# Kernel optimization log

Hardware: AMD Instinct MI355X
Metric: run time of the kernel (lower is better)

Reference implementation:

```python
import jax, jax.numpy as jnp
import numpy as np

NC, NX, NY = 32, 512, 512
N_LOC = 100000


def setup_inputs() -> dict:
    key = jax.random.key(0)
    k1, k2 = jax.random.split(key)
    x = jax.random.normal(k1, (8, NC, NX, NY), dtype=jnp.float32)
    kernel = jnp.zeros((1, NC, NX, NY), dtype=jnp.float32)
    variable_kernel = jax.random.normal(k2, (N_LOC,), dtype=jnp.float32)
    # unique flat indices into the (NC, NX, NY) kernel volume (cluster locations)
    rng = np.random.default_rng(0)
    loc_idx = jnp.asarray(rng.choice(NC * NX * NY, N_LOC, replace=False).astype(np.int64))
    return {"x": x, "kernel": kernel, "variable_kernel": variable_kernel, "loc_idx": loc_idx}


def fill_kernel(kernel, variable_kernel, loc_idx):
    # scatter ReLU'd trainable values into the sparse PSF locations
    k0 = kernel[0].reshape(-1).at[loc_idx].set(jax.nn.relu(variable_kernel))
    return k0.reshape(NC, NX, NY)


def disperse_all_orders(x, k):
    # per-channel circular convolution with the multi-order dispersion PSF,
    # summed over spectral channels onto the sensor: (b, nx, ny)
    Xf = jnp.fft.rfft2(x, axes=(-2, -1))          # (b, nc, nx, ny//2+1)
    Kf = jnp.fft.rfft2(k, axes=(-2, -1))          # (nc, nx, ny//2+1)
    Yf = jnp.sum(Xf * Kf[None], axis=1)           # (b, nx, ny//2+1)
    return jnp.fft.irfft2(Yf, s=(NX, NY), axes=(-2, -1))


def reference(x, kernel, variable_kernel, loc_idx):
    k = fill_kernel(kernel, variable_kernel, loc_idx)
    return disperse_all_orders(x, k)
```

## Files before the change

### kernel.cpp

```cpp
#include <hip/hip_runtime.h>
#include <cstdint>

#define NXX 512
#define NYY 512
#define NCH 32
#define NB  8
#define NU  257
#define IMG_CPLX (NU*NXX)
#define PIX (NXX*NYY)

__device__ __forceinline__ uint32_t f2bf(float f){
  uint32_t u = __float_as_uint(f);
  return (u + 0x7FFFu + ((u >> 16) & 1u)) >> 16;
}
__device__ __forceinline__ float bf2f(uint32_t h){ return __uint_as_float(h << 16); }
__device__ __forceinline__ uint32_t packbf(float re, float im){ return f2bf(re) | (f2bf(im) << 16); }

#define WAIT_LGKM() asm volatile("s_waitcnt lgkmcnt(0)" ::: "memory")

__device__ __forceinline__ void cmul(float& zr, float& zi, float wr, float wi){
  float r = zr*wr - zi*wi;
  zi = zr*wi + zi*wr;
  zr = r;
}

template<int DIR>
__device__ __forceinline__ void bfly8(float* xr, float* xi){
  const float S = 0.70710678118654752440f;
  float er0=xr[0]+xr[4], ei0=xi[0]+xi[4];
  float er1=xr[1]+xr[5], ei1=xi[1]+xi[5];
  float er2=xr[2]+xr[6], ei2=xi[2]+xi[6];
  float er3=xr[3]+xr[7], ei3=xi[3]+xi[7];
  float or0=xr[0]-xr[4], oi0=xi[0]-xi[4];
  float or1=xr[1]-xr[5], oi1=xi[1]-xi[5];
  float or2=xr[2]-xr[6], oi2=xi[2]-xi[6];
  float or3=xr[3]-xr[7], oi3=xi[3]-xi[7];
  float p0r=er0+er2, p0i=ei0+ei2;
  float p1r=er0-er2, p1i=ei0-ei2;
  float q0r=er1+er3, q0i=ei1+ei3;
  float q1r=er1-er3, q1i=ei1-ei3;
  float w4r, w4i;
  if (DIR<0){ w4r=q1i; w4i=-q1r; } else { w4r=-q1i; w4i=q1r; }
  xr[0]=p0r+q0r; xi[0]=p0i+q0i;
  xr[4]=p0r-q0r; xi[4]=p0i-q0i;
  xr[2]=p1r+w4r; xi[2]=p1i+w4i;
  xr[6]=p1r-w4r; xi[6]=p1i-w4i;
  float f1r,f1i,f2r,f2i,f3r,f3i;
  if (DIR<0){
    f1r=S*(or1+oi1); f1i=S*(oi1-or1);
    f2r=oi2;         f2i=-or2;
    f3r=S*(oi3-or3); f3i=-S*(or3+oi3);
  } else {
    f1r=S*(or1-oi1);  f1i=S*(or1+oi1);
    f2r=-oi2;         f2i=or2;
    f3r=-S*(or3+oi3); f3i=S*(or3-oi3);
  }
  float g0r=or0+f2r, g0i=oi0+f2i;
  float g1r=or0-f2r, g1i=oi0-f2i;
  float h0r=f1r+f3r, h0i=f1i+f3i;
  float h1r=f1r-f3r, h1i=f1i-f3i;
  float v4r, v4i;
  if (DIR<0){ v4r=h1i; v4i=-h1r; } else { v4r=-h1i; v4i=h1r; }
  xr[1]=g0r+h0r; xi[1]=g0i+h0i;
  xr[5]=g0r-h0r; xi[5]=g0i-h0i;
  xr[3]=g1r+v4r; xi[3]=g1i+v4i;
  xr[7]=g1r-v4r; xi[7]=g1i-v4i;
}

__device__ __forceinline__ void make_tw(int t, float* t1r, float* t1i, float* t2r, float* t2i){
  const float TP = 6.283185307179586476925f;
  float s, c;
  sincosf(-TP * (float)t * (1.0f/512.0f), &s, &c);
  t1r[0]=1.0f; t1i[0]=0.0f;
  #pragma unroll
  for (int k=1;k<8;k++){ t1r[k]=t1r[k-1]*c - t1i[k-1]*s; t1i[k]=t1r[k-1]*s + t1i[k-1]*c; }
  sincosf(-TP * (float)(t>>3) * (1.0f/64.0f), &s, &c);
  t2r[0]=1.0f; t2i[0]=0.0f;
  #pragma unroll
  for (int k=1;k<8;k++){ t2r[k]=t2r[k-1]*c - t2i[k-1]*s; t2i[k]=t2r[k-1]*s + t2i[k-1]*c; }
}

template<int DIR>
__device__ __forceinline__ void fft512(float* ar, float* ai, float* sre, float* sim, int t,
    const float* t1r, const float* t1i, const float* t2r, const float* t2i){
  bfly8<DIR>(ar, ai);
  #pragma unroll
  for (int k=1;k<8;k++){ cmul(ar[k], ai[k], t1r[k], (DIR<0)? t1i[k] : -t1i[k]); }
  #pragma unroll
  for (int k=0;k<8;k++){ int d = 8*t + k; d += (d>>5); sre[d]=ar[k]; sim[d]=ai[k]; }
  WAIT_LGKM();
  #pragma unroll
  for (int j=0;j<8;j++){ int s2 = t + (j<<6); s2 += (s2>>5); ar[j]=sre[s2]; ai[j]=sim[s2]; }
  WAIT_LGKM();
  bfly8<DIR>(ar, ai);
  #pragma unroll
  for (int k=1;k<8;k++){ cmul(ar[k], ai[k], t2r[k], (DIR<0)? t2i[k] : -t2i[k]); }
  #pragma unroll
  for (int k=0;k<8;k++){ int d = (t&7) + ((t>>3)<<6) + (k<<3); d += (d>>5); sre[d]=ar[k]; sim[d]=ai[k]; }
  WAIT_LGKM();
  #pragma unroll
  for (int j=0;j<8;j++){ int s2 = t + (j<<6); s2 += (s2>>5); ar[j]=sre[s2]; ai[j]=sim[s2]; }
  WAIT_LGKM();
  bfly8<DIR>(ar, ai);
}

__device__ __forceinline__ void stage_col_bf16(const uint32_t* __restrict__ col, float* S, int t,
                                               float* ar, float* ai){
  const uint4* c4 = (const uint4*)col;
  uint4 a = c4[t], b = c4[64+t];
  uint32_t wa[4]={a.x,a.y,a.z,a.w}, wb[4]={b.x,b.y,b.z,b.w};
  #pragma unroll
  for (int q=0;q<4;q++){
    int e=4*t+q,   d =e +(e >>5);  S[d ]=__uint_as_float(wa[q]);
    int e2=e+256,  d2=e2+(e2>>5);  S[d2]=__uint_as_float(wb[q]);
  }
  WAIT_LGKM();
  #pragma unroll
  for (int j=0;j<8;j++){ int s2=t+(j<<6); s2+=(s2>>5);
    uint32_t v=__float_as_uint(S[s2]); ar[j]=bf2f(v&0xFFFFu); ai[j]=bf2f(v>>16); }
  WAIT_LGKM();
}

__global__ __launch_bounds__(256) void k_zero(uint4* __restrict__ p, int n4){
  int stride = gridDim.x * 256;
  for (int i = blockIdx.x*256 + threadIdx.x; i < n4; i += stride)
    p[i] = make_uint4(0u,0u,0u,0u);
}

__global__ void k_scatter(const float* __restrict__ vk, const int* __restrict__ loc,
                          uint16_t* __restrict__ kbuf, int n){
  int i = blockIdx.x*256 + threadIdx.x;
  if (i < n){ float v = vk[i]; v = v > 0.0f ? v : 0.0f; kbuf[loc[i]] = (uint16_t)f2bf(v); }
}

template<int BF16>
__global__ __launch_bounds__(512) void k_p1(const void* __restrict__ srcv,
                                            uint32_t* __restrict__ dst){
  __shared__ float sre[8][528], sim[8][528];
  __shared__ uint32_t staged[NU*33];
  const int tid = threadIdx.x;
  const int w = tid >> 6, t = tid & 63;
  const int img = blockIdx.x >> 4;
  const int rblock = (blockIdx.x & 15) << 5;
  float t1r[8],t1i[8],t2r[8],t2i[8];
  make_tw(t, t1r,t1i,t2r,t2i);
  float* S = sre[w];
  float* T = sim[w];
  #pragma unroll
  for (int p=0; p<2; p++){
    const int il = (w<<2) + (p<<1);
    float ar[8], ai[8];
    if (BF16){
      const uint16_t* base = (const uint16_t*)srcv + (size_t)img*PIX + (size_t)(rblock + il)*NYY;
      const uint4* A4 = (const uint4*)base;
      uint4 a = A4[t], b = A4[64+t];
      uint32_t wa[4]={a.x,a.y,a.z,a.w}, wb[4]={b.x,b.y,b.z,b.w};
      #pragma unroll
      for (int q=0;q<4;q++){
        int e0=8*t+2*q, e1=e0+1;
        int d0=e0+(e0>>5), d1=e1+(e1>>5);
        S[d0]=bf2f(wa[q]&0xFFFFu); S[d1]=bf2f(wa[q]>>16);
        T[d0]=bf2f(wb[q]&0xFFFFu); T[d1]=bf2f(wb[q]>>16);
      }
      WAIT_LGKM();
      #pragma unroll
      for (int j=0;j<8;j++){ int s2=t+(j<<6); s2+=(s2>>5); ar[j]=S[s2]; ai[j]=T[s2]; }
      WAIT_LGKM();
    } else {
      const float* rowA = (const float*)srcv + (size_t)img*PIX + (size_t)(rblock + il)*NYY;
      const float4* A4 = (const float4*)rowA;
      float4 a0=A4[t], a1=A4[64+t], b0=A4[128+t], b1=A4[192+t];
      ((float4*)S)[t]=a0; ((float4*)S)[64+t]=a1;
      ((float4*)T)[t]=b0; ((float4*)T)[64+t]=b1;
      WAIT_LGKM();
      #pragma unroll
      for (int j=0;j<8;j++){ ar[j]=S[t+(j<<6)]; ai[j]=T[t+(j<<6)]; }
      WAIT_LGKM();
    }
    fft512<-1>(ar,ai,S,T,t,t1r,t1i,t2r,t2i);
    #pragma unroll
    for (int k=0;k<8;k++){ int d = t+(k<<6); d += (d>>5); S[d]=ar[k]; T[d]=ai[k]; }
    WAIT_LGKM();
    #pragma unroll
    for (int k=0;k<5;k++){
      int u = t + (k<<6);
      if (u < NU){
        int e2 = (512 - u) & 511;
        int du = u + (u>>5), d2 = e2 + (e2>>5);
        float zur=S[du], zui=T[du];
        float zvr=S[d2], zvi=T[d2];
        float Ar=0.5f*(zur+zvr), Ai=0.5f*(zui-zvi);
        float Br=0.5f*(zui+zvi), Bi=0.5f*(zvr-zur);
        staged[u*33 + il]     = packbf(Ar,Ai);
        staged[u*33 + il + 1] = packbf(Br,Bi);
      }
    }
    WAIT_LGKM();
  }
  __syncthreads();
  uint32_t* ob = dst + (size_t)img*IMG_CPLX;
  for (int e = tid; e < NU*32; e += 512){
    int u = e >> 5, il2 = e & 31;
    ob[(size_t)u*NXX + rblock + il2] = staged[u*33 + il2];
  }
}

__global__ __launch_bounds__(512) void k_p2k(uint32_t* __restrict__ rtk){
  __shared__ float sre[8][528], sim[8][528];
  const int w = threadIdx.x >> 6, t = threadIdx.x & 63;
  const int fid = blockIdx.x*8 + w;
  const int c = fid / NU, u = fid % NU;
  float t1r[8],t1i[8],t2r[8],t2i[8];
  make_tw(t, t1r,t1i,t2r,t2i);
  uint32_t* col = rtk + (size_t)c*IMG_CPLX + (size_t)u*NXX;
  float ar[8], ai[8];
  stage_col_bf16(col, sre[w], t, ar, ai);
  fft512<-1>(ar,ai,sre[w],sim[w],t,t1r,t1i,t2r,t2i);
  #pragma unroll
  for (int k=0;k<8;k++){ col[t+(k<<6)] = packbf(ar[k], ai[k]); }
}

__global__ __launch_bounds__(512) void k_p3(const uint32_t* __restrict__ rtx,
    const uint32_t* __restrict__ rtk, uint32_t* __restrict__ y3, int b0, int gsh){
  __shared__ float sre[8][528], sim[8][528];
  __shared__ float redr[8][512], redi[8][512];
  const int tid = threadIdx.x;
  const int w = tid >> 6, t = tid & 63;
  const int u  = blockIdx.x >> gsh;
  const int bl = blockIdx.x & ((1<<gsh)-1);
  float t1r[8],t1i[8],t2r[8],t2i[8];
  make_tw(t, t1r,t1i,t2r,t2i);
  float accr[8], acci[8];
  #pragma unroll
  for (int k=0;k<8;k++){ accr[k]=0.0f; acci[k]=0.0f; }
  #pragma unroll
  for (int cc=0; cc<4; cc++){
    const int c = (w<<2) + cc;
    const uint32_t* xc = rtx + ((size_t)(bl*NCH + c))*IMG_CPLX + (size_t)u*NXX;
    const uint32_t* kc = rtk + (size_t)c*IMG_CPLX + (size_t)u*NXX;
    uint32_t kv[8];
    #pragma unroll
    for (int j=0;j<8;j++){ kv[j]=kc[t+(j<<6)]; }
    float ar[8], ai[8];
    stage_col_bf16(xc, sre[w], t, ar, ai);
    fft512<-1>(ar,ai,sre[w],sim[w],t,t1r,t1i,t2r,t2i);
    #pragma unroll
    for (int k=0;k<8;k++){
      float kr=bf2f(kv[k] & 0xFFFFu), ki=bf2f(kv[k] >> 16);
      accr[k] += ar[k]*kr - ai[k]*ki;
      acci[k] += ar[k]*ki + ai[k]*kr;
    }
  }
  #pragma unroll
  for (int k=0;k<8;k++){ redr[w][t+(k<<6)] = accr[k]; redi[w][t+(k<<6)] = acci[k]; }
  __syncthreads();
  const float sc = 1.0f/262144.0f;
  float sr=0.0f, si=0.0f;
  #pragma unroll
  for (int ww=0; ww<8; ww++){ sr += redr[ww][tid]; si += redi[ww][tid]; }
  redr[0][tid] = sr*sc; redi[0][tid] = si*sc;
  __syncthreads();
  if (w==0){
    float ar[8], ai[8];
    #pragma unroll
    for (int j=0;j<8;j++){ ar[j]=redr[0][t+(j<<6)]; ai[j]=redi[0][t+(j<<6)]; }
    fft512<1>(ar,ai,sre[0],sim[0],t,t1r,t1i,t2r,t2i);
    uint32_t* yc = y3 + ((size_t)(b0+bl)*NU + u)*NXX;
    #pragma unroll
    for (int k=0;k<8;k++){ yc[t+(k<<6)] = packbf(ar[k], ai[k]); }
  }
}

__global__ __launch_bounds__(512) void k_p4(const uint32_t* __restrict__ y3,
                                            float* __restrict__ out){
  __shared__ float sre[8][528], sim[8][528];
  __shared__ uint32_t sta[NU*17];
  const int tid = threadIdx.x, w = tid>>6, t = tid&63;
  const int b = blockIdx.x >> 5;
  const int i0 = (blockIdx.x & 31) << 4;
  const uint32_t* yb = y3 + (size_t)b*IMG_CPLX;
  for (int e = tid; e < NU*16; e += 512){
    int u = e >> 4, il = e & 15;
    sta[u*17 + il] = yb[(size_t)u*NXX + i0 + il];
  }
  __syncthreads();
  float t1r[8],t1i[8],t2r[8],t2i[8];
  make_tw(t, t1r,t1i,t2r,t2i);
  float ar[8], ai[8];
  #pragma unroll
  for (int j=0;j<8;j++){
    int e = t + (j<<6);
    if (e <= 256){
      uint32_t pa_ = sta[e*17 + 2*w], pb_ = sta[e*17 + 2*w + 1];
      float Ar=bf2f(pa_&0xFFFFu), Ai=bf2f(pa_>>16);
      float Br=bf2f(pb_&0xFFFFu), Bi=bf2f(pb_>>16);
      ar[j] = Ar - Bi; ai[j] = Ai + Br;
    } else {
      int ep = 512 - e;
      uint32_t pa_ = sta[ep*17 + 2*w], pb_ = sta[ep*17 + 2*w + 1];
      float Ar=bf2f(pa_&0xFFFFu), Ai=bf2f(pa_>>16);
      float Br=bf2f(pb_&0xFFFFu), Bi=bf2f(pb_>>16);
      ar[j] = Ar + Bi; ai[j] = Br - Ai;
    }
  }
  fft512<1>(ar,ai,sre[w],sim[w],t,t1r,t1i,t2r,t2i);
  float* ob = out + (size_t)b*PIX + (size_t)(i0 + 2*w)*NYY;
  #pragma unroll
  for (int k=0;k<8;k++){ int n = t+(k<<6); ob[n]=ar[k]; ob[NYY+n]=ai[k]; }
}

extern "C" void kernel_launch(void* const* d_in, const int* in_sizes, int n_in,
                              void* d_out, int out_size, void* d_ws, size_t ws_size,
                              hipStream_t stream) {
  const float* x  = (const float*)d_in[0];
  const float* vk = (const float*)d_in[2];
  const int*   loc= (const int*)d_in[3];
  float* out = (float*)d_out;
  char* ws = (char*)d_ws;
  const int n_loc = in_sizes[2];

  const size_t kbytes16 = (size_t)NCH*PIX*2;
  const size_t imgbytes = (size_t)IMG_CPLX*4;

  uint16_t* kbuf = (uint16_t*)ws;
  uint32_t* y3   = (uint32_t*)ws;
  uint32_t* rtk  = (uint32_t*)(ws + kbytes16);
  uint32_t* rtx  = rtk + (size_t)NCH*IMG_CPLX;

  int G = 8;
  while (G > 1 && kbytes16 + (size_t)(NCH + NCH*G)*imgbytes > ws_size) G >>= 1;
  const int gsh = (G==8)?3:((G==4)?2:((G==2)?1:0));

  k_zero<<<2048, 256, 0, stream>>>((uint4*)kbuf, (int)(kbytes16/16));
  k_scatter<<<(n_loc+255)/256, 256, 0, stream>>>(vk, loc, kbuf, n_loc);
  k_p1<1><<<NCH*16, 512, 0, stream>>>(kbuf, rtk);
  k_p2k<<<(NCH*NU)/8, 512, 0, stream>>>(rtk);
  for (int b0 = 0; b0 < NB; b0 += G){
    k_p1<0><<<G*NCH*16, 512, 0, stream>>>(x + (size_t)b0*NCH*PIX, rtx);
    k_p3<<<NU<<gsh, 512, 0, stream>>>(rtx, rtk, y3, b0, gsh);
  }
  k_p4<<<NB*32, 512, 0, stream>>>(y3, out);
}
```

Measured before the change: 196.5 us.

## Load FFT inputs directly from global memory and shrink batch group size

Replaces the LDS staging of input rows and columns (vectorized global load, shared-memory write, then strided read) with direct strided global loads into registers in k_p1, k_p2k and k_p3. This removes LDS round trips and their waitcnt barriers, but the global loads become less vectorized and less coalesced. The batch group G drops from 8 to 2, so the p1/p3 pair runs four times over a smaller workspace. That may keep intermediates cache-resident, at the cost of more launches and lower per-launch parallelism.

```diff
diff --git a/kernel.cpp b/kernel.cpp
--- a/kernel.cpp
+++ b/kernel.cpp
@@ -104,23 +104,6 @@
   bfly8<DIR>(ar, ai);
 }
 
-__device__ __forceinline__ void stage_col_bf16(const uint32_t* __restrict__ col, float* S, int t,
-                                               float* ar, float* ai){
-  const uint4* c4 = (const uint4*)col;
-  uint4 a = c4[t], b = c4[64+t];
-  uint32_t wa[4]={a.x,a.y,a.z,a.w}, wb[4]={b.x,b.y,b.z,b.w};
-  #pragma unroll
-  for (int q=0;q<4;q++){
-    int e=4*t+q,   d =e +(e >>5);  S[d ]=__uint_as_float(wa[q]);
-    int e2=e+256,  d2=e2+(e2>>5);  S[d2]=__uint_as_float(wb[q]);
-  }
-  WAIT_LGKM();
-  #pragma unroll
-  for (int j=0;j<8;j++){ int s2=t+(j<<6); s2+=(s2>>5);
-    uint32_t v=__float_as_uint(S[s2]); ar[j]=bf2f(v&0xFFFFu); ai[j]=bf2f(v>>16); }
-  WAIT_LGKM();
-}
-
 __global__ __launch_bounds__(256) void k_zero(uint4* __restrict__ p, int n4){
   int stride = gridDim.x * 256;
   for (int i = blockIdx.x*256 + threadIdx.x; i < n4; i += stride)
@@ -168,14 +151,8 @@
       WAIT_LGKM();
     } else {
       const float* rowA = (const float*)srcv + (size_t)img*PIX + (size_t)(rblock + il)*NYY;
-      const float4* A4 = (const float4*)rowA;
-      float4 a0=A4[t], a1=A4[64+t], b0=A4[128+t], b1=A4[192+t];
-      ((float4*)S)[t]=a0; ((float4*)S)[64+t]=a1;
-      ((float4*)T)[t]=b0; ((float4*)T)[64+t]=b1;
-      WAIT_LGKM();
       #pragma unroll
-      for (int j=0;j<8;j++){ ar[j]=S[t+(j<<6)]; ai[j]=T[t+(j<<6)]; }
-      WAIT_LGKM();
+      for (int j=0;j<8;j++){ ar[j]=rowA[t+(j<<6)]; ai[j]=rowA[NYY + t + (j<<6)]; }
     }
     fft512<-1>(ar,ai,S,T,t,t1r,t1i,t2r,t2i);
     #pragma unroll
@@ -214,7 +191,8 @@
   make_tw(t, t1r,t1i,t2r,t2i);
   uint32_t* col = rtk + (size_t)c*IMG_CPLX + (size_t)u*NXX;
   float ar[8], ai[8];
-  stage_col_bf16(col, sre[w], t, ar, ai);
+  #pragma unroll
+  for (int j=0;j<8;j++){ uint32_t v = col[t+(j<<6)]; ar[j]=bf2f(v & 0xFFFFu); ai[j]=bf2f(v >> 16); }
   fft512<-1>(ar,ai,sre[w],sim[w],t,t1r,t1i,t2r,t2i);
   #pragma unroll
   for (int k=0;k<8;k++){ col[t+(k<<6)] = packbf(ar[k], ai[k]); }
@@ -238,11 +216,12 @@
     const int c = (w<<2) + cc;
     const uint32_t* xc = rtx + ((size_t)(bl*NCH + c))*IMG_CPLX + (size_t)u*NXX;
     const uint32_t* kc = rtk + (size_t)c*IMG_CPLX + (size_t)u*NXX;
-    uint32_t kv[8];
-    #pragma unroll
-    for (int j=0;j<8;j++){ kv[j]=kc[t+(j<<6)]; }
+    uint32_t xv[8], kv[8];
+    #pragma unroll
+    for (int j=0;j<8;j++){ xv[j]=xc[t+(j<<6)]; kv[j]=kc[t+(j<<6)]; }
     float ar[8], ai[8];
-    stage_col_bf16(xc, sre[w], t, ar, ai);
+    #pragma unroll
+    for (int j=0;j<8;j++){ ar[j]=bf2f(xv[j] & 0xFFFFu); ai[j]=bf2f(xv[j] >> 16); }
     fft512<-1>(ar,ai,sre[w],sim[w],t,t1r,t1i,t2r,t2i);
     #pragma unroll
     for (int k=0;k<8;k++){
@@ -327,9 +306,9 @@
   uint32_t* rtk  = (uint32_t*)(ws + kbytes16);
   uint32_t* rtx  = rtk + (size_t)NCH*IMG_CPLX;
 
-  int G = 8;
+  int G = 2;
   while (G > 1 && kbytes16 + (size_t)(NCH + NCH*G)*imgbytes > ws_size) G >>= 1;
-  const int gsh = (G==8)?3:((G==4)?2:((G==2)?1:0));
+  const int gsh = (G==2)?1:0;
 
   k_zero<<<2048, 256, 0, stream>>>((uint4*)kbuf, (int)(kbytes16/16));
   k_scatter<<<(n_loc+255)/256, 256, 0, stream>>>(vk, loc, kbuf, n_loc);
```

Measured after the change: 235.7 us. 20.0% more time.
